# Optimization experiments

Measured on AMD Instinct MI355X. Metric: run time of the kernel, lower is better.

## Reference

```python
import jax, jax.numpy as jnp
import numpy as np

N_HEAD = 16
NEG = -10000.0


def setup_inputs() -> dict:
    key = jax.random.key(0)
    k1, k2, k3 = jax.random.split(key, 3)
    B, S, NX = 2, 2048, 1024
    x = jax.random.normal(k1, (B, S, NX), dtype=jnp.float32)
    # Conv1D weights: y = x @ W + b (HF Conv1D stores weight as [in, out])
    w_attn = jax.random.normal(k2, (NX, 3 * NX), dtype=jnp.float32) * 0.02
    b_attn = jnp.zeros((3 * NX,), dtype=jnp.float32)
    w_proj = jax.random.normal(k3, (NX, NX), dtype=jnp.float32) * 0.02
    b_proj = jnp.zeros((NX,), dtype=jnp.float32)
    return {"x": x, "w_attn": w_attn, "b_attn": b_attn,
            "w_proj": w_proj, "b_proj": b_proj}


def reference(x, w_attn, b_attn, w_proj, b_proj):
    B, S, NX = x.shape
    H = N_HEAD
    D = NX // H  # head dim
    qkv = x @ w_attn + b_attn                      # [B, S, 3*NX]
    q, k, v = jnp.split(qkv, 3, axis=-1)
    # split heads -> [B, H, S, D]
    q = q.reshape(B, S, H, D).transpose(0, 2, 1, 3)
    k = k.reshape(B, S, H, D).transpose(0, 2, 1, 3)
    v = v.reshape(B, S, H, D).transpose(0, 2, 1, 3)
    # scores [B, H, S, S], scaled (scale=True)
    w = jnp.einsum('bhqd,bhkd->bhqk', q, k) / jnp.sqrt(jnp.asarray(D, x.dtype))
    # causal additive mask exactly as the torch code: w*b + NEG*(1-b)
    bias = jnp.tril(jnp.ones((S, S), dtype=x.dtype))[None, None]  # [1,1,S,S]
    w = w * bias + NEG * (1.0 - bias)
    w = jax.nn.softmax(w, axis=-1)
    a = jnp.einsum('bhqk,bhkd->bhqd', w, v)        # [B, H, S, D]
    a = a.transpose(0, 2, 1, 3).reshape(B, S, NX)  # merge heads
    return a @ w_proj + b_proj
```

## Files before the change

kernel.cpp:

```cpp
#include <hip/hip_runtime.h>
#include <cstdint>
#include <cstddef>


typedef __bf16 bf16;
typedef __bf16 bf16x8 __attribute__((ext_vector_type(8)));
typedef __bf16 bf16x4 __attribute__((ext_vector_type(4)));
typedef short s16x4 __attribute__((ext_vector_type(4)));
typedef float f32x4 __attribute__((ext_vector_type(4)));

#define MFMA16(a, b, c) __builtin_amdgcn_mfma_f32_16x16x32_bf16(a, b, c, 0, 0, 0)
#define MFMA16K16(a, b, c) __builtin_amdgcn_mfma_f32_16x16x16bf16_1k(a, b, c, 0, 0, 0)

typedef const __attribute__((address_space(1))) void* gas_ptr;
typedef __attribute__((address_space(3))) void* las_ptr;
__device__ __forceinline__ void async16(const void* g, void* l) {
    __builtin_amdgcn_global_load_lds((gas_ptr)g, (las_ptr)l, 16, 0, 0);
}
__device__ __forceinline__ float exp2f_fast(float x) { return __builtin_amdgcn_exp2f(x); }

__global__ __launch_bounds__(256) void prep_kernel(const float* __restrict__ x, bf16* __restrict__ xb,
                                                   const float* __restrict__ wa, bf16* __restrict__ wTa,
                                                   const float* __restrict__ wp, bf16* __restrict__ wTp) {
    __shared__ float tile[32][33];
    const int bid = blockIdx.x, tid = threadIdx.x;
    if (bid < 4096) {
        int i = (bid * 256 + tid) * 4;
        float4 v = *reinterpret_cast<const float4*>(x + i);
        bf16x4 o;
        o[0] = (bf16)v.x; o[1] = (bf16)v.y; o[2] = (bf16)v.z; o[3] = (bf16)v.w;
        *reinterpret_cast<bf16x4*>(xb + i) = o;
        return;
    }
    const float* in; bf16* out; int N, t;
    if (bid < 7168) { t = bid - 4096; in = wa; out = wTa; N = 3072; }
    else            { t = bid - 7168; in = wp; out = wTp; N = 1024; }
    const int K = 1024;
    int bx = t % (N >> 5), by = t / (N >> 5);
    int n0 = bx * 32, k0 = by * 32, tx = tid & 31, ty = tid >> 5;
#pragma unroll
    for (int i = 0; i < 32; i += 8)
        tile[ty + i][tx] = in[(size_t)(k0 + ty + i) * N + n0 + tx];
    __syncthreads();
#pragma unroll
    for (int i = 0; i < 32; i += 8)
        out[(size_t)(n0 + ty + i) * K + k0 + tx] = (bf16)tile[tx][ty + i];
}

template <int OUT_BF16>
__global__ __launch_bounds__(256) void gemm_kernel(const bf16* __restrict__ A,
                                                   const bf16* __restrict__ Bt,
                                                   const float* __restrict__ bias,
                                                   void* __restrict__ Cout,
                                                   int M, int N, int K) {
    __shared__ bf16 Alds[2][128 * 32];
    __shared__ bf16 Blds[2][128 * 32];
    const int tid = threadIdx.x;
    const int w = tid >> 6, l = tid & 63;
    const int lane16 = l & 15, quad = l >> 4;
    const int wr = w >> 1, wc = w & 1;
    const int row0 = blockIdx.y * 128, col0 = blockIdx.x * 128;

    const int e = tid * 8;
    const int sr = e >> 5, sc = e & 31;

    f32x4 zero4 = {0.f, 0.f, 0.f, 0.f};
    f32x4 acc[4][4];
#pragma unroll
    for (int i = 0; i < 4; ++i)
#pragma unroll
        for (int j = 0; j < 4; ++j) acc[i][j] = zero4;

#pragma unroll
    for (int ch = 0; ch < 2; ++ch) {
        async16(A + (size_t)(row0 + ch * 64 + sr) * K + sc, &Alds[0][ch * 2048 + e]);
        async16(Bt + (size_t)(col0 + ch * 64 + sr) * K + sc, &Blds[0][ch * 2048 + e]);
    }

    const int niter = K >> 5;
    for (int it = 0; it < niter; ++it) {
        const int cur = it & 1;
        __syncthreads();
        if (it + 1 < niter) {
            const int k1 = (it + 1) << 5;
#pragma unroll
            for (int ch = 0; ch < 2; ++ch) {
                async16(A + (size_t)(row0 + ch * 64 + sr) * K + k1 + sc, &Alds[cur ^ 1][ch * 2048 + e]);
                async16(Bt + (size_t)(col0 + ch * 64 + sr) * K + k1 + sc, &Blds[cur ^ 1][ch * 2048 + e]);
            }
        }
        bf16x8 af[4], bfr[4];
#pragma unroll
        for (int i = 0; i < 4; ++i) {
            af[i] = *reinterpret_cast<const bf16x8*>(&Alds[cur][(64 * wr + 16 * i + lane16) * 32 + quad * 8]);
            bfr[i] = *reinterpret_cast<const bf16x8*>(&Blds[cur][(64 * wc + 16 * i + lane16) * 32 + quad * 8]);
        }
#pragma unroll
        for (int i = 0; i < 4; ++i)
#pragma unroll
            for (int j = 0; j < 4; ++j) acc[i][j] = MFMA16(af[i], bfr[j], acc[i][j]);
    }

#pragma unroll
    for (int i = 0; i < 4; ++i)
#pragma unroll
        for (int j = 0; j < 4; ++j)
#pragma unroll
            for (int r = 0; r < 4; ++r) {
                int row = row0 + 64 * wr + 16 * i + quad * 4 + r;
                int col = col0 + 64 * wc + 16 * j + lane16;
                float v = acc[i][j][r] + bias[col];
                if (OUT_BF16)
                    reinterpret_cast<bf16*>(Cout)[(size_t)row * N + col] = (bf16)v;
                else
                    reinterpret_cast<float*>(Cout)[(size_t)row * N + col] = v;
            }
}

template <int OUT_BF16>
__global__ __launch_bounds__(256) void gemm64k_kernel(const bf16* __restrict__ A,
                                                      const bf16* __restrict__ Bt,
                                                      const float* __restrict__ bias,
                                                      void* __restrict__ Cout,
                                                      int M, int N, int K) {
    __shared__ bf16 Alds[2][64 * 64];
    __shared__ bf16 Blds[2][128 * 64];
    const int tid = threadIdx.x;
    const int w = tid >> 6, l = tid & 63;
    const int lane16 = l & 15, quad = l >> 4;
    const int wr = w >> 1, wc = w & 1;
    const int row0 = blockIdx.y * 64, col0 = blockIdx.x * 128;

    f32x4 zero4 = {0.f, 0.f, 0.f, 0.f};
    f32x4 acc[2][4];
#pragma unroll
    for (int i = 0; i < 2; ++i)
#pragma unroll
        for (int j = 0; j < 4; ++j) acc[i][j] = zero4;

    auto stage = [&](int buf, int k0) {
#pragma unroll
        for (int c = 0; c < 2; ++c) {
            int idx = c * 256 + tid;
            int r = idx >> 3, cc = idx & 7, gc = cc ^ (r & 7);
            async16(A + (size_t)(row0 + r) * K + k0 + gc * 8, &Alds[buf][idx * 8]);
        }
#pragma unroll
        for (int c = 0; c < 4; ++c) {
            int idx = c * 256 + tid;
            int r = idx >> 3, cc = idx & 7, gc = cc ^ (r & 7);
            async16(Bt + (size_t)(col0 + r) * K + k0 + gc * 8, &Blds[buf][idx * 8]);
        }
    };

    stage(0, 0);
    const int niter = K >> 6;
    for (int it = 0; it < niter; ++it) {
        const int cur = it & 1;
        __syncthreads();
        if (it + 1 < niter) stage(cur ^ 1, (it + 1) << 6);
        bf16x8 af[2][2], bfr[4][2];
#pragma unroll
        for (int i = 0; i < 2; ++i) {
            int r = 32 * wr + 16 * i + lane16;
#pragma unroll
            for (int ks = 0; ks < 2; ++ks) {
                int cc = (quad + 4 * ks) ^ (r & 7);
                af[i][ks] = *reinterpret_cast<const bf16x8*>(&Alds[cur][r * 64 + cc * 8]);
            }
        }
#pragma unroll
        for (int j = 0; j < 4; ++j) {
            int r = 64 * wc + 16 * j + lane16;
#pragma unroll
            for (int ks = 0; ks < 2; ++ks) {
                int cc = (quad + 4 * ks) ^ (r & 7);
                bfr[j][ks] = *reinterpret_cast<const bf16x8*>(&Blds[cur][r * 64 + cc * 8]);
            }
        }
#pragma unroll
        for (int ks = 0; ks < 2; ++ks)
#pragma unroll
            for (int i = 0; i < 2; ++i)
#pragma unroll
                for (int j = 0; j < 4; ++j) acc[i][j] = MFMA16(af[i][ks], bfr[j][ks], acc[i][j]);
    }

#pragma unroll
    for (int i = 0; i < 2; ++i)
#pragma unroll
        for (int j = 0; j < 4; ++j)
#pragma unroll
            for (int r = 0; r < 4; ++r) {
                int row = row0 + 32 * wr + 16 * i + quad * 4 + r;
                int col = col0 + 64 * wc + 16 * j + lane16;
                float v = acc[i][j][r] + bias[col];
                if (OUT_BF16)
                    reinterpret_cast<bf16*>(Cout)[(size_t)row * N + col] = (bf16)v;
                else
                    reinterpret_cast<float*>(Cout)[(size_t)row * N + col] = v;
            }
}

__global__ __launch_bounds__(256, 3) void attn_kernel(const bf16* __restrict__ qkv,
                                                      bf16* __restrict__ aout) {
    const int S = 2048;
    const int bh = blockIdx.x;
    const int b = bh >> 4, h = bh & 15;
    const int rr = blockIdx.y >> 3, jj = blockIdx.y & 7;
    const int qt = (rr == 0) ? (31 - jj) : (rr == 1) ? (16 + jj) : (rr == 2) ? (15 - jj) : jj;
    const int nkt = qt + 1;
    const int tid = threadIdx.x, w = tid >> 6, l = tid & 63;
    const int lane16 = l & 15, quad = l >> 4;

    __shared__ __align__(16) char smem[64 * 72 * 2 * 2];
    bf16* Klds = (bf16*)smem;
    bf16* Vt = (bf16*)(smem + 64 * 72 * 2);
    float* Ored = (float*)smem;
    __shared__ float Lred[4][4][16];

    const bf16* base = qkv + (size_t)b * S * 3072;
    const float qscale = 0.125f * 1.4426950408889634f;
    const float NEGs = -10000.0f * 1.4426950408889634f;

    bf16x8 qf[4][2];
#pragma unroll
    for (int q4 = 0; q4 < 4; ++q4) {
        const bf16* qp = base + (size_t)(qt * 64 + 16 * q4 + lane16) * 3072 + h * 64;
#pragma unroll
        for (int dh = 0; dh < 2; ++dh) {
            bf16x8 t = *reinterpret_cast<const bf16x8*>(qp + dh * 32 + quad * 8);
#pragma unroll
            for (int j = 0; j < 8; ++j) t[j] = (bf16)((float)t[j] * qscale);
            qf[q4][dh] = t;
        }
    }

    f32x4 zero4 = {0.f, 0.f, 0.f, 0.f};
    f32x4 o[4][4];
#pragma unroll
    for (int i = 0; i < 4; ++i)
#pragma unroll
        for (int j = 0; j < 4; ++j) o[i][j] = zero4;
    float lsum[4] = {0.f, 0.f, 0.f, 0.f};

    const int kr = tid >> 3, kc = (tid & 7) * 8;
    const int vp = tid & 31, vd = (tid >> 5) * 8;
    bf16x8 kreg0, kreg1, vreg0, vreg1;
    auto load_tile = [&](int kt) {
        const bf16* tb = base + (size_t)(kt * 64) * 3072;
        kreg0 = *reinterpret_cast<const bf16x8*>(tb + (size_t)kr * 3072 + 1024 + h * 64 + kc);
        kreg1 = *reinterpret_cast<const bf16x8*>(tb + (size_t)(32 + kr) * 3072 + 1024 + h * 64 + kc);
        vreg0 = *reinterpret_cast<const bf16x8*>(tb + (size_t)(2 * vp) * 3072 + 2048 + h * 64 + vd);
        vreg1 = *reinterpret_cast<const bf16x8*>(tb + (size_t)(2 * vp + 1) * 3072 + 2048 + h * 64 + vd);
    };

    load_tile(0);
    for (int kt = 0; kt < nkt; ++kt) {
        __syncthreads();
        *reinterpret_cast<bf16x8*>(&Klds[kr * 72 + kc]) = kreg0;
        *reinterpret_cast<bf16x8*>(&Klds[(32 + kr) * 72 + kc]) = kreg1;
#pragma unroll
        for (int j = 0; j < 8; ++j) {
            union { bf16 h2[2]; uint32_t u; } pk;
            pk.h2[0] = vreg0[j]; pk.h2[1] = vreg1[j];
            *reinterpret_cast<uint32_t*>(&Vt[(vd + j) * 72 + 2 * vp]) = pk.u;
        }
        __syncthreads();
        if (kt + 1 < nkt) load_tile(kt + 1);

        bf16x8 ka0 = *reinterpret_cast<const bf16x8*>(&Klds[(16 * w + lane16) * 72 + quad * 8]);
        bf16x8 ka1 = *reinterpret_cast<const bf16x8*>(&Klds[(16 * w + lane16) * 72 + 32 + quad * 8]);
        f32x4 st[4];
#pragma unroll
        for (int q4 = 0; q4 < 4; ++q4) {
            f32x4 z = zero4;
            z = MFMA16(ka0, qf[q4][0], z);
            z = MFMA16(ka1, qf[q4][1], z);
            st[q4] = z;
        }

        if (kt == qt) {
            const int key0 = kt * 64 + 16 * w + quad * 4;
#pragma unroll
            for (int q4 = 0; q4 < 4; ++q4) {
                const int q = qt * 64 + 16 * q4 + lane16;
#pragma unroll
                for (int r = 0; r < 4; ++r)
                    if (key0 + r > q) st[q4][r] = NEGs;
            }
        }

        s16x4 pA[4];
#pragma unroll
        for (int q4 = 0; q4 < 4; ++q4) {
            union { bf16 b[4]; s16x4 s; } pk;
            float rs = 0.f;
#pragma unroll
            for (int r = 0; r < 4; ++r) {
                float pv = exp2f_fast(st[q4][r]);
                rs += pv;
                pk.b[r] = (bf16)pv;
            }
            lsum[q4] += rs;
            pA[q4] = pk.s;
        }

#pragma unroll
        for (int df = 0; df < 4; ++df) {
            s16x4 vB = *reinterpret_cast<const s16x4*>(&Vt[(df * 16 + lane16) * 72 + 16 * w + quad * 4]);
#pragma unroll
            for (int q4 = 0; q4 < 4; ++q4)
                o[q4][df] = MFMA16K16(pA[q4], vB, o[q4][df]);
        }
    }

#pragma unroll
    for (int q4 = 0; q4 < 4; ++q4) {
        float lw = lsum[q4];
        lw += __shfl_xor(lw, 16, 64);
        lw += __shfl_xor(lw, 32, 64);
        lsum[q4] = lw;
    }
    if (quad == 0) {
#pragma unroll
        for (int q4 = 0; q4 < 4; ++q4) Lred[w][q4][lane16] = lsum[q4];
    }
    __syncthreads();
    float invw = Lred[0][w][lane16] + Lred[1][w][lane16] + Lred[2][w][lane16] + Lred[3][w][lane16];
    invw = 1.0f / invw;
    float invq[4];
#pragma unroll
    for (int r = 0; r < 4; ++r) invq[r] = __shfl(invw, quad * 4 + r, 64);

#pragma unroll
    for (int df = 0; df < 4; ++df) {
        __syncthreads();
#pragma unroll
        for (int q4 = 0; q4 < 4; ++q4)
#pragma unroll
            for (int r = 0; r < 4; ++r)
                Ored[(w * 64 + 16 * q4 + 4 * quad + r) * 17 + lane16] = o[q4][df][r];
        __syncthreads();
#pragma unroll
        for (int r = 0; r < 4; ++r) {
            int qrow = 16 * w + 4 * quad + r;
            float s = Ored[(0 * 64 + qrow) * 17 + lane16] + Ored[(1 * 64 + qrow) * 17 + lane16] +
                      Ored[(2 * 64 + qrow) * 17 + lane16] + Ored[(3 * 64 + qrow) * 17 + lane16];
            int row = qt * 64 + qrow;
            aout[(size_t)(b * S + row) * 1024 + h * 64 + 16 * df + lane16] =
                (bf16)(s * invq[r]);
        }
    }
}

extern "C" void kernel_launch(void* const* d_in, const int* in_sizes, int n_in,
                              void* d_out, int out_size, void* d_ws, size_t ws_size,
                              hipStream_t stream) {
    const float* x      = (const float*)d_in[0];
    const float* w_attn = (const float*)d_in[1];
    const float* b_attn = (const float*)d_in[2];
    const float* w_proj = (const float*)d_in[3];
    const float* b_proj = (const float*)d_in[4];
    float* out = (float*)d_out;
    char* ws = (char*)d_ws;

    const int Mtok = 4096, NX = 1024, N3 = 3072;
    bf16* xb   = (bf16*)(ws);
    bf16* wTa  = (bf16*)(ws + ((size_t)8 << 20));
    bf16* wTp  = (bf16*)(ws + ((size_t)14 << 20));
    bf16* qkv  = (bf16*)(ws + ((size_t)16 << 20));
    bf16* abuf = (bf16*)(ws + ((size_t)40 << 20));

    prep_kernel<<<dim3(8192), 256, 0, stream>>>(x, xb, w_attn, wTa, w_proj, wTp);
    gemm_kernel<1><<<dim3(N3 / 128, Mtok / 128), 256, 0, stream>>>(xb, wTa, b_attn, qkv, Mtok, N3, NX);
    attn_kernel<<<dim3(32, 32), 256, 0, stream>>>(qkv, abuf);
    gemm64k_kernel<0><<<dim3(NX / 128, Mtok / 64), 256, 0, stream>>>(abuf, wTp, b_proj, out, Mtok, NX, NX);
}
```

Baseline: 173.4 us.

## Split long causal attention query tiles across two blocks with a reduce pass

```diff
diff --git a/kernel.cpp b/kernel.cpp
--- a/kernel.cpp
+++ b/kernel.cpp
@@ -202,14 +202,26 @@
             }
 }
 
-__global__ __launch_bounds__(256, 3) void attn_kernel(const bf16* __restrict__ qkv,
-                                                      bf16* __restrict__ aout) {
+__global__ __launch_bounds__(256, 6) void attn_kernel(const bf16* __restrict__ qkv,
+                                                      bf16* __restrict__ aout,
+                                                      float* __restrict__ opart,
+                                                      float* __restrict__ lpart) {
     const int S = 2048;
     const int bh = blockIdx.x;
     const int b = bh >> 4, h = bh & 15;
-    const int rr = blockIdx.y >> 3, jj = blockIdx.y & 7;
-    const int qt = (rr == 0) ? (31 - jj) : (rr == 1) ? (16 + jj) : (rr == 2) ? (15 - jj) : jj;
-    const int nkt = qt + 1;
+    const int y = blockIdx.y;
+    int qt, w0, w1, sp;
+    bool partial;
+    if (y < 32) {
+        qt = 16 + (y >> 1);
+        sp = y & 1;
+        int nkt = qt + 1, h0 = (nkt + 1) >> 1;
+        w0 = sp ? h0 : 0;
+        w1 = sp ? nkt : h0;
+        partial = true;
+    } else {
+        qt = 47 - y; sp = 0; w0 = 0; w1 = qt + 1; partial = false;
+    }
     const int tid = threadIdx.x, w = tid >> 6, l = tid & 63;
     const int lane16 = l & 15, quad = l >> 4;
 
@@ -255,8 +267,8 @@
         vreg1 = *reinterpret_cast<const bf16x8*>(tb + (size_t)(2 * vp + 1) * 3072 + 2048 + h * 64 + vd);
     };
 
-    load_tile(0);
-    for (int kt = 0; kt < nkt; ++kt) {
+    load_tile(w0);
+    for (int kt = w0; kt < w1; ++kt) {
         __syncthreads();
         *reinterpret_cast<bf16x8*>(&Klds[kr * 72 + kc]) = kreg0;
         *reinterpret_cast<bf16x8*>(&Klds[(32 + kr) * 72 + kc]) = kreg1;
@@ -267,7 +279,7 @@
             *reinterpret_cast<uint32_t*>(&Vt[(vd + j) * 72 + 2 * vp]) = pk.u;
         }
         __syncthreads();
-        if (kt + 1 < nkt) load_tile(kt + 1);
+        if (kt + 1 < w1) load_tile(kt + 1);
 
         bf16x8 ka0 = *reinterpret_cast<const bf16x8*>(&Klds[(16 * w + lane16) * 72 + quad * 8]);
         bf16x8 ka1 = *reinterpret_cast<const bf16x8*>(&Klds[(16 * w + lane16) * 72 + 32 + quad * 8]);
@@ -294,13 +306,13 @@
         s16x4 pA[4];
 #pragma unroll
         for (int q4 = 0; q4 < 4; ++q4) {
-            union { bf16 b[4]; s16x4 s; } pk;
+            union { bf16 bb[4]; s16x4 s; } pk;
             float rs = 0.f;
 #pragma unroll
             for (int r = 0; r < 4; ++r) {
                 float pv = exp2f_fast(st[q4][r]);
                 rs += pv;
-                pk.b[r] = (bf16)pv;
+                pk.bb[r] = (bf16)pv;
             }
             lsum[q4] += rs;
             pA[q4] = pk.s;
@@ -327,8 +339,12 @@
         for (int q4 = 0; q4 < 4; ++q4) Lred[w][q4][lane16] = lsum[q4];
     }
     __syncthreads();
-    float invw = Lred[0][w][lane16] + Lred[1][w][lane16] + Lred[2][w][lane16] + Lred[3][w][lane16];
-    invw = 1.0f / invw;
+    float ltot = Lred[0][w][lane16] + Lred[1][w][lane16] + Lred[2][w][lane16] + Lred[3][w][lane16];
+    const int ridb = (bh << 10) + (qt - 16) * 64;
+    if (partial) {
+        if (quad == 0) lpart[(size_t)sp * 32768 + ridb + 16 * w + lane16] = ltot;
+    }
+    float invw = 1.0f / ltot;
     float invq[4];
 #pragma unroll
     for (int r = 0; r < 4; ++r) invq[r] = __shfl(invw, quad * 4 + r, 64);
@@ -347,11 +363,33 @@
             int qrow = 16 * w + 4 * quad + r;
             float s = Ored[(0 * 64 + qrow) * 17 + lane16] + Ored[(1 * 64 + qrow) * 17 + lane16] +
                       Ored[(2 * 64 + qrow) * 17 + lane16] + Ored[(3 * 64 + qrow) * 17 + lane16];
-            int row = qt * 64 + qrow;
-            aout[(size_t)(b * S + row) * 1024 + h * 64 + 16 * df + lane16] =
-                (bf16)(s * invq[r]);
-        }
-    }
+            if (partial) {
+                opart[((size_t)sp * 32768 + ridb + qrow) * 64 + 16 * df + lane16] = s;
+            } else {
+                int row = qt * 64 + qrow;
+                aout[(size_t)(b * S + row) * 1024 + h * 64 + 16 * df + lane16] =
+                    (bf16)(s * invq[r]);
+            }
+        }
+    }
+}
+
+__global__ __launch_bounds__(256) void reduce_kernel(const float* __restrict__ opart,
+                                                     const float* __restrict__ lpart,
+                                                     bf16* __restrict__ abuf) {
+    int i = blockIdx.x * 256 + threadIdx.x;
+    int rid = i >> 4, d4 = (i & 15) * 4;
+    float4 a = *reinterpret_cast<const float4*>(opart + (size_t)rid * 64 + d4);
+    float4 c = *reinterpret_cast<const float4*>(opart + ((size_t)32768 + rid) * 64 + d4);
+    float inv = 1.0f / (lpart[rid] + lpart[32768 + rid]);
+    int bh = rid >> 10, qr = (rid & 1023) + 1024;
+    int bb = bh >> 4, hh = bh & 15;
+    bf16x4 o;
+    o[0] = (bf16)((a.x + c.x) * inv);
+    o[1] = (bf16)((a.y + c.y) * inv);
+    o[2] = (bf16)((a.z + c.z) * inv);
+    o[3] = (bf16)((a.w + c.w) * inv);
+    *reinterpret_cast<bf16x4*>(abuf + (size_t)(bb * 2048 + qr) * 1024 + hh * 64 + d4) = o;
 }
 
 extern "C" void kernel_launch(void* const* d_in, const int* in_sizes, int n_in,
@@ -366,14 +404,17 @@
     char* ws = (char*)d_ws;
 
     const int Mtok = 4096, NX = 1024, N3 = 3072;
-    bf16* xb   = (bf16*)(ws);
-    bf16* wTa  = (bf16*)(ws + ((size_t)8 << 20));
-    bf16* wTp  = (bf16*)(ws + ((size_t)14 << 20));
-    bf16* qkv  = (bf16*)(ws + ((size_t)16 << 20));
-    bf16* abuf = (bf16*)(ws + ((size_t)40 << 20));
+    bf16* xb    = (bf16*)(ws);
+    bf16* wTa   = (bf16*)(ws + ((size_t)8 << 20));
+    bf16* wTp   = (bf16*)(ws + ((size_t)14 << 20));
+    bf16* qkv   = (bf16*)(ws + ((size_t)16 << 20));
+    bf16* abuf  = (bf16*)(ws + ((size_t)40 << 20));
+    float* opart = (float*)(ws + ((size_t)48 << 20));
+    float* lpart = (float*)(ws + ((size_t)64 << 20));
 
     prep_kernel<<<dim3(8192), 256, 0, stream>>>(x, xb, w_attn, wTa, w_proj, wTp);
     gemm_kernel<1><<<dim3(N3 / 128, Mtok / 128), 256, 0, stream>>>(xb, wTa, b_attn, qkv, Mtok, N3, NX);
-    attn_kernel<<<dim3(32, 32), 256, 0, stream>>>(qkv, abuf);
+    attn_kernel<<<dim3(32, 48), 256, 0, stream>>>(qkv, abuf, opart, lpart);
+    reduce_kernel<<<dim3(32768 * 16 / 256), 256, 0, stream>>>(opart, lpart, abuf);
     gemm64k_kernel<0><<<dim3(NX / 128, Mtok / 64), 256, 0, stream>>>(abuf, wTp, b_proj, out, Mtok, NX, NX);
 }
```

Measured after the change: 464.5 us. 168% more time.
